# Performance work log

Hardware: AMD Instinct MI355X
Metric: run time of the kernel (lower is better)

The kernel has to match this reference:

```python
import jax, jax.numpy as jnp
import numpy as np

N_NODES = 10000
N_EDGES = 160000
LN_EPS = 1e-5
BN_EPS = 1e-5


def _leaky(x, slope=0.2):
    return jnp.where(x >= 0, x, slope * x)


def _gat_conv(x, edge_index, W, att_src, att_dst, bias, concat):
    # x: [N, Din]; W: [Din, H*C]; att_*: [H, C]
    H, C = att_src.shape
    h = (x @ W).reshape(-1, H, C)                       # [N, H, C]
    a_src = jnp.einsum('nhc,hc->nh', h, att_src)        # [N, H]
    a_dst = jnp.einsum('nhc,hc->nh', h, att_dst)
    src, dst = edge_index[0], edge_index[1]
    logits = _leaky(a_src[src] + a_dst[dst], 0.2)       # [E, H]
    # segment softmax over incoming edges of each dst node
    m = jax.ops.segment_max(logits, dst, num_segments=N_NODES)
    e = jnp.exp(logits - m[dst])
    denom = jax.ops.segment_sum(e, dst, num_segments=N_NODES)
    alpha = e / denom[dst]                              # [E, H]
    msg = h[src] * alpha[:, :, None]                    # [E, H, C]
    out = jax.ops.segment_sum(msg, dst, num_segments=N_NODES)  # [N, H, C]
    if concat:
        out = out.reshape(-1, H * C)
    else:
        out = out.mean(axis=1)
    return out + bias


def setup_inputs() -> dict:
    key = jax.random.key(0)
    ks = jax.random.split(key, 10)
    d_in, H, C = 128, 8, 64
    W = H * C  # 512
    return {
        'x': jax.random.normal(ks[0], (N_NODES, d_in), jnp.float32),
        'edge_index': jax.random.randint(ks[1], (2, N_EDGES), 0, N_NODES, jnp.int64),
        'ft_W': jax.random.normal(ks[2], (d_in, W), jnp.float32) * (1.0 / np.sqrt(d_in)),
        'ft_b': jnp.zeros((W,), jnp.float32),
        'ln_g': jnp.ones((W,), jnp.float32),
        'ln_b': jnp.zeros((W,), jnp.float32),
        'W1': jax.random.normal(ks[3], (W, H * C), jnp.float32) * (1.0 / np.sqrt(W)),
        'att_src1': jax.random.normal(ks[4], (H, C), jnp.float32) * 0.1,
        'att_dst1': jax.random.normal(ks[5], (H, C), jnp.float32) * 0.1,
        'b1': jnp.zeros((W,), jnp.float32),
        'bn_g': jnp.ones((W,), jnp.float32),
        'bn_b': jnp.zeros((W,), jnp.float32),
        'bn_mean': jnp.zeros((W,), jnp.float32),
        'bn_var': jnp.ones((W,), jnp.float32),
        'W2': jax.random.normal(ks[6], (W, H * 2), jnp.float32) * (1.0 / np.sqrt(W)),
        'att_src2': jax.random.normal(ks[7], (H, 2), jnp.float32) * 0.1,
        'att_dst2': jax.random.normal(ks[8], (H, 2), jnp.float32) * 0.1,
        'b2': jnp.zeros((2,), jnp.float32),
    }


def reference(x, edge_index, ft_W, ft_b, ln_g, ln_b, W1, att_src1, att_dst1, b1,
              bn_g, bn_b, bn_mean, bn_var, W2, att_src2, att_dst2, b2):
    # feature transform: Linear -> LayerNorm -> LeakyReLU(0.2)
    h = x @ ft_W + ft_b
    mu = h.mean(axis=-1, keepdims=True)
    var = h.var(axis=-1, keepdims=True)
    h = (h - mu) * jax.lax.rsqrt(var + LN_EPS) * ln_g + ln_b
    h = _leaky(h, 0.2)
    # GAT layer 1 (concat heads) -> BatchNorm (eval) -> ReLU  (dropout = identity in eval)
    h = _gat_conv(h, edge_index, W1, att_src1, att_dst1, b1, concat=True)
    h = (h - bn_mean) * jax.lax.rsqrt(bn_var + BN_EPS) * bn_g + bn_b
    h = jax.nn.relu(h)
    # GAT layer 2 (mean heads) -> logits [N, 2]
    logits = _gat_conv(h, edge_index, W2, att_src2, att_dst2, b2, concat=False)
    return logits
```

## Files before the change

### kernel.cpp

```cpp
#include <hip/hip_runtime.h>
#include <hip/hip_bf16.h>
#include <math.h>

#define N_NODES 10000
#define N_EDGES 160000
#define DIN 128
#define DW 512
#define NHEAD 8
#define NC 64
#define MPAD 10112
#define GEMM_BLKS 316

typedef unsigned short ushort_t;
typedef __attribute__((ext_vector_type(8))) short bf16x8;
typedef __attribute__((ext_vector_type(8))) unsigned short us8;
typedef __attribute__((ext_vector_type(4))) float f32x4;

__device__ inline ushort_t f2bf(float v) {
    unsigned u = __builtin_bit_cast(unsigned, v);
    return (ushort_t)((u + 0x7fff + ((u >> 16) & 1)) >> 16);
}
__device__ inline float bf2f(ushort_t h) {
    return __builtin_bit_cast(float, (unsigned)h << 16);
}

__device__ __forceinline__ size_t swz_idx(int rb, int r, int kp, int nkt) {
    int kt = kp >> 6, kc = kp & 63;
    return ((size_t)(rb * nkt + kt)) * 8192 + r * 64 + (kc ^ ((r & 7) << 3));
}

__device__ __forceinline__ void gld16(const ushort_t* g, ushort_t* l) {
    __builtin_amdgcn_global_load_lds(
        (const __attribute__((address_space(1))) void*)g,
        (__attribute__((address_space(3))) void*)l, 16, 0, 0);
}

__global__ void k_prep(const float* __restrict__ x, const float* __restrict__ ftW,
                       const float* __restrict__ W1f,
                       ushort_t* __restrict__ Ax, ushort_t* __restrict__ Bx,
                       ushort_t* __restrict__ B1,
                       int* __restrict__ cnt, int* __restrict__ cursor) {
    int bid = blockIdx.x, t = threadIdx.x;
    if (bid < 632) {
        int gid = bid * 256 + t;
        int n = gid >> 4, k0 = (gid & 15) * 8;
        float v[8];
        if (n < N_NODES) {
            #pragma unroll
            for (int u = 0; u < 8; u++) v[u] = x[n * DIN + k0 + u];
        } else {
            #pragma unroll
            for (int u = 0; u < 8; u++) v[u] = 0.f;
        }
        us8 hi, lo;
        #pragma unroll
        for (int u = 0; u < 8; u++) {
            ushort_t h = f2bf(v[u]);
            hi[u] = h;
            lo[u] = f2bf(v[u] - bf2f(h));
        }
        int rb = n >> 7, r = n & 127;
        *(us8*)(Ax + swz_idx(rb, r, k0, 4)) = hi;
        *(us8*)(Ax + swz_idx(rb, r, 128 + k0, 4)) = lo;
    } else if (bid < 888) {
        int i = (bid - 632) * 256 + t;
        int n = i >> 7, k = i & 127;
        ushort_t h = f2bf(ftW[k * DW + n]);
        int cb = n >> 7, rc = n & 127;
        Bx[swz_idx(cb, rc, k, 4)] = h;
        Bx[swz_idx(cb, rc, 128 + k, 4)] = h;
    } else if (bid < 1912) {
        int i = (bid - 888) * 256 + t;
        int n = i >> 9, k = i & 511;
        ushort_t h = f2bf(W1f[k * DW + n]);
        int cb = n >> 7, rc = n & 127;
        B1[swz_idx(cb, rc, k, 16)] = h;
        B1[swz_idx(cb, rc, 512 + k, 16)] = h;
    } else {
        int i = (bid - 1912) * 256 + t;
        if (i < N_NODES) { cnt[i] = 0; cursor[i] = 0; }
    }
}

template<int KT, bool ATT, int EXTRA>
__global__ __launch_bounds__(512, 4) void k_tgemm(const ushort_t* __restrict__ A,
                                                  const ushort_t* __restrict__ Bm,
                                                  float* __restrict__ C,
                                                  ushort_t* __restrict__ Cb,
                                                  const float* __restrict__ asrc,
                                                  const float* __restrict__ adst,
                                                  float* __restrict__ aS,
                                                  float* __restrict__ aD,
                                                  const int* __restrict__ ei,
                                                  int* __restrict__ cnt,
                                                  const int* __restrict__ off,
                                                  int* __restrict__ cursor,
                                                  int* __restrict__ csrc) {
    __shared__ __align__(16) ushort_t As[2][8192];
    __shared__ __align__(16) ushort_t Bs[2][8192];
    int bid = blockIdx.x;
    if (bid >= GEMM_BLKS) {
        int e = (bid - GEMM_BLKS) * 512 + threadIdx.x;
        if (e < N_EDGES) {
            if (EXTRA == 1) {
                atomicAdd(&cnt[ei[N_EDGES + e]], 1);
            } else {
                int d = ei[N_EDGES + e];
                int p = off[d] + atomicAdd(&cursor[d], 1);
                csrc[p] = ei[e];
            }
        }
        return;
    }
    int bx = bid >> 2, by = bid & 3;
    int t = threadIdx.x, w = t >> 6, l = t & 63;
    int lm = l & 15, g = l >> 4;
    int wr = w >> 1, wc = w & 1;
    int rowbase = bx * 128;
    int colbase = by * 128;

    const ushort_t* Abase = A + (size_t)bx * KT * 8192 + t * 8;
    const ushort_t* Bbase = Bm + (size_t)by * KT * 8192 + t * 8;

    f32x4 acc[2][4];
    #pragma unroll
    for (int r = 0; r < 2; r++)
        #pragma unroll
        for (int c = 0; c < 4; c++) acc[r][c] = (f32x4){0.f, 0.f, 0.f, 0.f};

    {
        #pragma unroll
        for (int j = 0; j < 2; ++j) {
            gld16(Abase + j * 4096, &As[0][j * 4096 + t * 8]);
            gld16(Bbase + j * 4096, &Bs[0][j * 4096 + t * 8]);
        }
    }

    int p = 0;
    for (int kt = 0; kt < KT; ++kt) {
        __builtin_amdgcn_s_barrier();
        if (kt + 1 < KT) {
            const ushort_t* ga = Abase + (size_t)(kt + 1) * 8192;
            const ushort_t* gb = Bbase + (size_t)(kt + 1) * 8192;
            #pragma unroll
            for (int j = 0; j < 2; ++j) {
                gld16(ga + j * 4096, &As[p ^ 1][j * 4096 + t * 8]);
                gld16(gb + j * 4096, &Bs[p ^ 1][j * 4096 + t * 8]);
            }
            asm volatile("s_waitcnt vmcnt(4)" ::: "memory");
        } else {
            asm volatile("s_waitcnt vmcnt(0)" ::: "memory");
        }
        __builtin_amdgcn_s_barrier();
        const char* Ap = (const char*)As[p];
        const char* Bp = (const char*)Bs[p];
        #pragma unroll
        for (int ks = 0; ks < 2; ++ks) {
            bf16x8 af[2], bfr[4];
            #pragma unroll
            for (int r = 0; r < 2; ++r) {
                int row = wr * 32 + r * 16 + lm;
                af[r] = *(const bf16x8*)(Ap + row * 128 +
                                         ((ks * 64 + g * 16) ^ ((row & 7) << 4)));
            }
            #pragma unroll
            for (int c = 0; c < 4; ++c) {
                int col = wc * 64 + c * 16 + lm;
                bfr[c] = *(const bf16x8*)(Bp + col * 128 +
                                          ((ks * 64 + g * 16) ^ ((col & 7) << 4)));
            }
            #pragma unroll
            for (int r = 0; r < 2; ++r)
                #pragma unroll
                for (int c = 0; c < 4; ++c)
                    acc[r][c] = __builtin_amdgcn_mfma_f32_16x16x32_bf16(af[r], bfr[c], acc[r][c], 0, 0, 0);
        }
        p ^= 1;
    }

    if (!ATT) {
        #pragma unroll
        for (int r = 0; r < 2; ++r) {
            int row0 = rowbase + wr * 32 + r * 16 + g * 4;
            #pragma unroll
            for (int c = 0; c < 4; ++c) {
                int col = colbase + wc * 64 + c * 16 + lm;
                #pragma unroll
                for (int q = 0; q < 4; ++q)
                    if (row0 + q < N_NODES) C[(size_t)(row0 + q) * DW + col] = acc[r][c][q];
            }
        }
    } else {
        int h = 2 * by + wc;
        float asv[4], adv[4];
        #pragma unroll
        for (int c = 0; c < 4; ++c) {
            asv[c] = asrc[h * NC + c * 16 + lm];
            adv[c] = adst[h * NC + c * 16 + lm];
        }
        #pragma unroll
        for (int r = 0; r < 2; ++r) {
            int row0 = rowbase + wr * 32 + r * 16 + g * 4;
            #pragma unroll
            for (int c = 0; c < 4; ++c) {
                int col = colbase + wc * 64 + c * 16 + lm;
                #pragma unroll
                for (int q = 0; q < 4; ++q)
                    if (row0 + q < N_NODES) Cb[(size_t)(row0 + q) * DW + col] = f2bf(acc[r][c][q]);
            }
            #pragma unroll
            for (int q = 0; q < 4; ++q) {
                float ss = acc[r][0][q] * asv[0] + acc[r][1][q] * asv[1] +
                           acc[r][2][q] * asv[2] + acc[r][3][q] * asv[3];
                float dd = acc[r][0][q] * adv[0] + acc[r][1][q] * adv[1] +
                           acc[r][2][q] * adv[2] + acc[r][3][q] * adv[3];
                #pragma unroll
                for (int m = 1; m < 16; m <<= 1) {
                    ss += __shfl_xor(ss, m, 64);
                    dd += __shfl_xor(dd, m, 64);
                }
                int row = row0 + q;
                if (lm == 0 && row < N_NODES) {
                    aS[row * NHEAD + h] = ss;
                    aD[row * NHEAD + h] = dd;
                }
            }
        }
    }
}

__global__ __launch_bounds__(256) void k_ln_scan(const float* __restrict__ hpre,
                                                 const float* __restrict__ fb,
                                                 const float* __restrict__ g,
                                                 const float* __restrict__ beta,
                                                 ushort_t* __restrict__ h0big,
                                                 const int* __restrict__ cnt,
                                                 int* __restrict__ off) {
    __shared__ int ps[256];
    __shared__ float red[8];
    __shared__ __align__(16) ushort_t st[1024];
    int bid = blockIdx.x, t = threadIdx.x;
    if (bid == MPAD) {
        int base = t * 40;
        int loc[40];
        int s = 0;
        #pragma unroll
        for (int i = 0; i < 40; i++) {
            int idx = base + i;
            int v = idx < N_NODES ? cnt[idx] : 0;
            loc[i] = s; s += v;
        }
        ps[t] = s; __syncthreads();
        for (int o = 1; o < 256; o <<= 1) {
            int v = (t >= o) ? ps[t - o] : 0;
            __syncthreads();
            ps[t] += v;
            __syncthreads();
        }
        int pre = (t > 0) ? ps[t - 1] : 0;
        #pragma unroll
        for (int i = 0; i < 40; i++) {
            int idx = base + i;
            if (idx < N_NODES) off[idx] = pre + loc[i];
        }
        if (t == 255) off[N_NODES] = ps[255];
        return;
    }
    int n = bid;
    int rb = n >> 7, r = n & 127;
    if (n >= N_NODES) {
        if (t < 128) {
            int kp0 = t * 8;
            *(us8*)(h0big + ((size_t)(rb * 16 + (kp0 >> 6))) * 8192 + r * 64 +
                    ((kp0 & 63) ^ ((r & 7) << 3))) = (us8){0,0,0,0,0,0,0,0};
        }
        return;
    }
    float a0 = hpre[(size_t)n * DW + t] + fb[t];
    float a1 = hpre[(size_t)n * DW + t + 256] + fb[t + 256];
    float s = a0 + a1, sq = a0 * a0 + a1 * a1;
    for (int o = 32; o > 0; o >>= 1) { s += __shfl_down(s, o, 64); sq += __shfl_down(sq, o, 64); }
    int wid = t >> 6;
    if ((t & 63) == 0) { red[wid] = s; red[4 + wid] = sq; }
    __syncthreads();
    if (t == 0) {
        float ts = red[0] + red[1] + red[2] + red[3];
        float tq = red[4] + red[5] + red[6] + red[7];
        float mu = ts / DW;
        float var = tq / DW - mu * mu;
        red[0] = mu; red[1] = rsqrtf(var + 1e-5f);
    }
    __syncthreads();
    float mu = red[0], rs = red[1];
    float v0 = (a0 - mu) * rs * g[t] + beta[t];
    float v1 = (a1 - mu) * rs * g[t + 256] + beta[t + 256];
    v0 = v0 >= 0.f ? v0 : 0.2f * v0;
    v1 = v1 >= 0.f ? v1 : 0.2f * v1;
    ushort_t h0_ = f2bf(v0), l0_ = f2bf(v0 - bf2f(h0_));
    ushort_t h1_ = f2bf(v1), l1_ = f2bf(v1 - bf2f(h1_));
    st[t] = h0_;        st[256 + t] = h1_;
    st[512 + t] = l0_;  st[768 + t] = l1_;
    __syncthreads();
    if (t < 128) {
        int kp0 = t * 8;
        *(us8*)(h0big + ((size_t)(rb * 16 + (kp0 >> 6))) * 8192 + r * 64 +
                ((kp0 & 63) ^ ((r & 7) << 3))) = *(const us8*)(st + kp0);
    }
}

__global__ __launch_bounds__(256) void k_agg1csr(
    const int* __restrict__ csrc, const int* __restrict__ off,
    const ushort_t* __restrict__ h1b,
    const float* __restrict__ aS, const float* __restrict__ aD,
    const float* __restrict__ b1, const float* __restrict__ bnm,
    const float* __restrict__ bnv, const float* __restrict__ bng,
    const float* __restrict__ bnb, ushort_t* __restrict__ h2b)
{
    int n = blockIdx.x, t = threadIdx.x;
    int beg = off[n], end = off[n + 1];
    __shared__ float wls[64][NHEAD];
    __shared__ int   sls[64];
    __shared__ float aDn[NHEAD];
    __shared__ float dsum[NHEAD];
    if (t < NHEAD) { aDn[t] = aD[n * NHEAD + t]; dsum[t] = 0.f; }
    __syncthreads();
    float acc0 = 0.f, acc1 = 0.f, dpart = 0.f;
    int hA = t >> 5;
    for (int c = beg; c < end; c += 64) {
        int m = min(64, end - c);
        if (t < m) sls[t] = csrc[c + t];
        __syncthreads();
        for (int idx = t; idx < m * NHEAD; idx += 256) {
            int el = idx >> 3, h = idx & 7;
            float l = aS[sls[el] * NHEAD + h] + aDn[h];
            l = l >= 0.f ? l : 0.2f * l;
            float w = __expf(l);
            wls[el][h] = w;
            dpart += w;
        }
        __syncthreads();
        for (int el = 0; el < m; el++) {
            float w = wls[el][hA];
            unsigned v = *(const unsigned*)(h1b + (size_t)sls[el] * DW + 2 * t);
            acc0 += w * __builtin_bit_cast(float, v << 16);
            acc1 += w * __builtin_bit_cast(float, v & 0xffff0000u);
        }
        __syncthreads();
    }
    for (int o = 8; o < 64; o <<= 1) dpart += __shfl_down(dpart, o, 64);
    if ((t & 63) < NHEAD) atomicAdd(&dsum[t & 7], dpart);
    __syncthreads();
    float rd = dsum[hA] > 0.f ? 1.f / dsum[hA] : 0.f;
    int j0 = 2 * t, j1 = 2 * t + 1;
    float v0 = acc0 * rd + b1[j0];
    v0 = (v0 - bnm[j0]) * rsqrtf(bnv[j0] + 1e-5f) * bng[j0] + bnb[j0];
    v0 = v0 > 0.f ? v0 : 0.f;
    float v1 = acc1 * rd + b1[j1];
    v1 = (v1 - bnm[j1]) * rsqrtf(bnv[j1] + 1e-5f) * bng[j1] + bnb[j1];
    v1 = v1 > 0.f ? v1 : 0.f;
    unsigned pk = (unsigned)f2bf(v0) | ((unsigned)f2bf(v1) << 16);
    *(unsigned*)(h2b + (size_t)n * DW + 2 * t) = pk;
}

__global__ __launch_bounds__(256) void k_gemm2att(const ushort_t* __restrict__ h2b,
                                                  const float* __restrict__ W2,
                                                  const float* __restrict__ as2,
                                                  const float* __restrict__ ad2,
                                                  float* __restrict__ gout,
                                                  float* __restrict__ aS,
                                                  float* __restrict__ aD) {
    __shared__ float Ws[DW * 16];
    __shared__ float gl[16][16];
    __shared__ float a2[32];
    int t = threadIdx.x;
    for (int i = t; i < DW * 16; i += 256) Ws[i] = W2[i];
    if (t < 16) a2[t] = as2[t];
    else if (t < 32) a2[t] = ad2[t - 16];
    __syncthreads();
    int nb = blockIdx.x * 16;
    int nl = t >> 4, j = t & 15;
    const bf16x8* hr = (const bf16x8*)(h2b + (size_t)(nb + nl) * DW);
    float acc = 0.f;
    for (int ks = 0; ks < DW / 8; ks++) {
        bf16x8 v = hr[ks];
        #pragma unroll
        for (int u = 0; u < 8; u++)
            acc += bf2f((ushort_t)v[u]) * Ws[(ks * 8 + u) * 16 + j];
    }
    gout[(nb + nl) * 16 + j] = acc;
    gl[nl][j] = acc;
    __syncthreads();
    if (j < 8) {
        aS[(nb + nl) * NHEAD + j] = gl[nl][2 * j] * a2[2 * j] + gl[nl][2 * j + 1] * a2[2 * j + 1];
    } else {
        int h = j - 8;
        aD[(nb + nl) * NHEAD + h] = gl[nl][2 * h] * a2[16 + 2 * h] + gl[nl][2 * h + 1] * a2[16 + 2 * h + 1];
    }
}

__global__ __launch_bounds__(256) void k_agg2csr(
    const int* __restrict__ csrc, const int* __restrict__ off,
    const float* __restrict__ gbuf,
    const float* __restrict__ aS, const float* __restrict__ aD,
    const float* __restrict__ b2, float* __restrict__ outp)
{
    int t = threadIdx.x;
    int n = blockIdx.x * 4 + (t >> 6);
    int lane = t & 63;
    if (n >= N_NODES) return;
    int beg = off[n], end = off[n + 1];
    int j = lane & 15, slot = lane >> 4, h = j >> 1;
    float adn = aD[n * NHEAD + h];
    float acc = 0.f, den = 0.f;
    for (int c = beg + slot; c < end; c += 4) {
        int s = csrc[c];
        float l = aS[s * NHEAD + h] + adn;
        l = l >= 0.f ? l : 0.2f * l;
        float w = __expf(l);
        den += w;
        acc += w * gbuf[s * 16 + j];
    }
    acc += __shfl_down(acc, 16, 64); acc += __shfl_down(acc, 32, 64);
    den += __shfl_down(den, 16, 64); den += __shfl_down(den, 32, 64);
    float v = (lane < 16 && den > 0.f) ? acc / den : 0.f;
    v += __shfl_down(v, 2, 64);
    v += __shfl_down(v, 4, 64);
    v += __shfl_down(v, 8, 64);
    if (lane < 2) outp[n * 2 + lane] = v * 0.125f + b2[lane];
}

extern "C" void kernel_launch(void* const* d_in, const int* in_sizes, int n_in,
                              void* d_out, int out_size, void* d_ws, size_t ws_size,
                              hipStream_t stream) {
    const float* x    = (const float*)d_in[0];
    const int*   ei   = (const int*)d_in[1];
    const float* ftW  = (const float*)d_in[2];
    const float* ftb  = (const float*)d_in[3];
    const float* lng  = (const float*)d_in[4];
    const float* lnb  = (const float*)d_in[5];
    const float* W1   = (const float*)d_in[6];
    const float* as1  = (const float*)d_in[7];
    const float* ad1  = (const float*)d_in[8];
    const float* b1   = (const float*)d_in[9];
    const float* bng  = (const float*)d_in[10];
    const float* bnb  = (const float*)d_in[11];
    const float* bnm  = (const float*)d_in[12];
    const float* bnv  = (const float*)d_in[13];
    const float* W2   = (const float*)d_in[14];
    const float* as2  = (const float*)d_in[15];
    const float* ad2  = (const float*)d_in[16];
    const float* b2   = (const float*)d_in[17];
    float* out = (float*)d_out;

    float* F = (float*)d_ws;
    ushort_t* Ax    = (ushort_t*)(F + 0);
    float*    gbuf  = F + 0;
    ushort_t* Bx    = (ushort_t*)(F + 1294336);
    ushort_t* B1    = (ushort_t*)(F + 1359872);
    float*    hpre  = F + 1622016;
    ushort_t* h2b   = (ushort_t*)(F + 1622016);
    ushort_t* h0big = (ushort_t*)(F + 6799360);
    ushort_t* h1b   = (ushort_t*)(F + 11976704);
    float*    aS1   = F + 14536704;
    float*    aD1   = F + 14616704;
    int* cnt        = (int*)(F + 14696704);
    int* cursor     = (int*)(F + 14706704);
    int* off        = (int*)(F + 14716704);
    int* csrc       = (int*)(F + 14726705);

    k_prep<<<1952, 256, 0, stream>>>(x, ftW, W1, Ax, Bx, B1, cnt, cursor);
    k_tgemm<4, false, 1><<<GEMM_BLKS + 313, 512, 0, stream>>>(
        Ax, Bx, hpre, nullptr, nullptr, nullptr, nullptr, nullptr,
        ei, cnt, nullptr, nullptr, nullptr);
    k_ln_scan<<<MPAD + 1, 256, 0, stream>>>(hpre, ftb, lng, lnb, h0big, cnt, off);
    k_tgemm<16, true, 2><<<GEMM_BLKS + 313, 512, 0, stream>>>(
        h0big, B1, nullptr, h1b, as1, ad1, aS1, aD1,
        ei, nullptr, off, cursor, csrc);
    k_agg1csr<<<N_NODES, 256, 0, stream>>>(csrc, off, h1b, aS1, aD1, b1, bnm, bnv, bng, bnb, h2b);
    k_gemm2att<<<N_NODES / 16, 256, 0, stream>>>(h2b, W2, as2, ad2, gbuf, aS1, aD1);
    k_agg2csr<<<(N_NODES + 3) / 4, 256, 0, stream>>>(csrc, off, gbuf, aS1, aD1, b2, out);
}
```

Baseline: 126.1 us.

## Fuse layer-2 projection and attention scores into layer-1 aggregation kernel

```diff
diff --git a/kernel.cpp b/kernel.cpp
--- a/kernel.cpp
+++ b/kernel.cpp
@@ -271,8 +271,7 @@
     if (n >= N_NODES) {
         if (t < 128) {
             int kp0 = t * 8;
-            *(us8*)(h0big + ((size_t)(rb * 16 + (kp0 >> 6))) * 8192 + r * 64 +
-                    ((kp0 & 63) ^ ((r & 7) << 3))) = (us8){0,0,0,0,0,0,0,0};
+            *(us8*)(h0big + swz_idx(rb, r, kp0, 16)) = (us8){0,0,0,0,0,0,0,0};
         }
         return;
     }
@@ -303,18 +302,20 @@
     __syncthreads();
     if (t < 128) {
         int kp0 = t * 8;
-        *(us8*)(h0big + ((size_t)(rb * 16 + (kp0 >> 6))) * 8192 + r * 64 +
-                ((kp0 & 63) ^ ((r & 7) << 3))) = *(const us8*)(st + kp0);
-    }
-}
-
-__global__ __launch_bounds__(256) void k_agg1csr(
+        *(us8*)(h0big + swz_idx(rb, r, kp0, 16)) = *(const us8*)(st + kp0);
+    }
+}
+
+__global__ __launch_bounds__(256) void k_agg1g2(
     const int* __restrict__ csrc, const int* __restrict__ off,
     const ushort_t* __restrict__ h1b,
     const float* __restrict__ aS, const float* __restrict__ aD,
     const float* __restrict__ b1, const float* __restrict__ bnm,
     const float* __restrict__ bnv, const float* __restrict__ bng,
-    const float* __restrict__ bnb, ushort_t* __restrict__ h2b)
+    const float* __restrict__ bnb,
+    const float* __restrict__ W2, const float* __restrict__ as2,
+    const float* __restrict__ ad2,
+    float* __restrict__ gbuf, float* __restrict__ aS2, float* __restrict__ aD2)
 {
     int n = blockIdx.x, t = threadIdx.x;
     int beg = off[n], end = off[n + 1];
@@ -322,6 +323,9 @@
     __shared__ int   sls[64];
     __shared__ float aDn[NHEAD];
     __shared__ float dsum[NHEAD];
+    __shared__ float h2row[DW];
+    __shared__ float pr[16][17];
+    __shared__ float gl[16];
     if (t < NHEAD) { aDn[t] = aD[n * NHEAD + t]; dsum[t] = 0.f; }
     __syncthreads();
     float acc0 = 0.f, acc1 = 0.f, dpart = 0.f;
@@ -358,43 +362,29 @@
     float v1 = acc1 * rd + b1[j1];
     v1 = (v1 - bnm[j1]) * rsqrtf(bnv[j1] + 1e-5f) * bng[j1] + bnb[j1];
     v1 = v1 > 0.f ? v1 : 0.f;
-    unsigned pk = (unsigned)f2bf(v0) | ((unsigned)f2bf(v1) << 16);
-    *(unsigned*)(h2b + (size_t)n * DW + 2 * t) = pk;
-}
-
-__global__ __launch_bounds__(256) void k_gemm2att(const ushort_t* __restrict__ h2b,
-                                                  const float* __restrict__ W2,
-                                                  const float* __restrict__ as2,
-                                                  const float* __restrict__ ad2,
-                                                  float* __restrict__ gout,
-                                                  float* __restrict__ aS,
-                                                  float* __restrict__ aD) {
-    __shared__ float Ws[DW * 16];
-    __shared__ float gl[16][16];
-    __shared__ float a2[32];
-    int t = threadIdx.x;
-    for (int i = t; i < DW * 16; i += 256) Ws[i] = W2[i];
-    if (t < 16) a2[t] = as2[t];
-    else if (t < 32) a2[t] = ad2[t - 16];
-    __syncthreads();
-    int nb = blockIdx.x * 16;
-    int nl = t >> 4, j = t & 15;
-    const bf16x8* hr = (const bf16x8*)(h2b + (size_t)(nb + nl) * DW);
-    float acc = 0.f;
-    for (int ks = 0; ks < DW / 8; ks++) {
-        bf16x8 v = hr[ks];
-        #pragma unroll
-        for (int u = 0; u < 8; u++)
-            acc += bf2f((ushort_t)v[u]) * Ws[(ks * 8 + u) * 16 + j];
-    }
-    gout[(nb + nl) * 16 + j] = acc;
-    gl[nl][j] = acc;
-    __syncthreads();
-    if (j < 8) {
-        aS[(nb + nl) * NHEAD + j] = gl[nl][2 * j] * a2[2 * j] + gl[nl][2 * j + 1] * a2[2 * j + 1];
-    } else {
-        int h = j - 8;
-        aD[(nb + nl) * NHEAD + h] = gl[nl][2 * h] * a2[16 + 2 * h] + gl[nl][2 * h + 1] * a2[16 + 2 * h + 1];
+    h2row[j0] = v0;
+    h2row[j1] = v1;
+    __syncthreads();
+    int j = t & 15, seg = t >> 4;
+    const float* wp = W2 + (seg * 32) * 16 + j;
+    float part = 0.f;
+    #pragma unroll 8
+    for (int k = 0; k < 32; k++) part += h2row[seg * 32 + k] * wp[k * 16];
+    pr[seg][j] = part;
+    __syncthreads();
+    if (t < 16) {
+        float accg = 0.f;
+        #pragma unroll
+        for (int s2 = 0; s2 < 16; s2++) accg += pr[s2][t];
+        gl[t] = accg;
+        gbuf[n * 16 + t] = accg;
+    }
+    __syncthreads();
+    if (t < 8) {
+        aS2[n * NHEAD + t] = gl[2 * t] * as2[2 * t] + gl[2 * t + 1] * as2[2 * t + 1];
+    } else if (t < 16) {
+        int h = t - 8;
+        aD2[n * NHEAD + h] = gl[2 * h] * ad2[2 * h] + gl[2 * h + 1] * ad2[2 * h + 1];
     }
 }
 
@@ -458,15 +448,16 @@
     ushort_t* Bx    = (ushort_t*)(F + 1294336);
     ushort_t* B1    = (ushort_t*)(F + 1359872);
     float*    hpre  = F + 1622016;
-    ushort_t* h2b   = (ushort_t*)(F + 1622016);
     ushort_t* h0big = (ushort_t*)(F + 6799360);
     ushort_t* h1b   = (ushort_t*)(F + 11976704);
     float*    aS1   = F + 14536704;
     float*    aD1   = F + 14616704;
-    int* cnt        = (int*)(F + 14696704);
-    int* cursor     = (int*)(F + 14706704);
-    int* off        = (int*)(F + 14716704);
-    int* csrc       = (int*)(F + 14726705);
+    float*    aS2   = F + 14696704;
+    float*    aD2   = F + 14776704;
+    int* cnt        = (int*)(F + 14856704);
+    int* cursor     = (int*)(F + 14866704);
+    int* off        = (int*)(F + 14876704);
+    int* csrc       = (int*)(F + 14886705);
 
     k_prep<<<1952, 256, 0, stream>>>(x, ftW, W1, Ax, Bx, B1, cnt, cursor);
     k_tgemm<4, false, 1><<<GEMM_BLKS + 313, 512, 0, stream>>>(
@@ -476,7 +467,8 @@
     k_tgemm<16, true, 2><<<GEMM_BLKS + 313, 512, 0, stream>>>(
         h0big, B1, nullptr, h1b, as1, ad1, aS1, aD1,
         ei, nullptr, off, cursor, csrc);
-    k_agg1csr<<<N_NODES, 256, 0, stream>>>(csrc, off, h1b, aS1, aD1, b1, bnm, bnv, bng, bnb, h2b);
-    k_gemm2att<<<N_NODES / 16, 256, 0, stream>>>(h2b, W2, as2, ad2, gbuf, aS1, aD1);
-    k_agg2csr<<<(N_NODES + 3) / 4, 256, 0, stream>>>(csrc, off, gbuf, aS1, aD1, b2, out);
-}
+    k_agg1g2<<<N_NODES, 256, 0, stream>>>(csrc, off, h1b, aS1, aD1,
+                                          b1, bnm, bnv, bng, bnb,
+                                          W2, as2, ad2, gbuf, aS2, aD2);
+    k_agg2csr<<<(N_NODES + 3) / 4, 256, 0, stream>>>(csrc, off, gbuf, aS2, aD2, b2, out);
+}
```

Measured after the change: 120.5 us. 1.05x faster.

## Split layer-1 aggregation per head with edge-parallel slots per node group

Applied to the files above, without the earlier changes.

```diff
diff --git a/kernel.cpp b/kernel.cpp
--- a/kernel.cpp
+++ b/kernel.cpp
@@ -271,8 +271,7 @@
     if (n >= N_NODES) {
         if (t < 128) {
             int kp0 = t * 8;
-            *(us8*)(h0big + ((size_t)(rb * 16 + (kp0 >> 6))) * 8192 + r * 64 +
-                    ((kp0 & 63) ^ ((r & 7) << 3))) = (us8){0,0,0,0,0,0,0,0};
+            *(us8*)(h0big + swz_idx(rb, r, kp0, 16)) = (us8){0,0,0,0,0,0,0,0};
         }
         return;
     }
@@ -303,12 +302,11 @@
     __syncthreads();
     if (t < 128) {
         int kp0 = t * 8;
-        *(us8*)(h0big + ((size_t)(rb * 16 + (kp0 >> 6))) * 8192 + r * 64 +
-                ((kp0 & 63) ^ ((r & 7) << 3))) = *(const us8*)(st + kp0);
-    }
-}
-
-__global__ __launch_bounds__(256) void k_agg1csr(
+        *(us8*)(h0big + swz_idx(rb, r, kp0, 16)) = *(const us8*)(st + kp0);
+    }
+}
+
+__global__ __launch_bounds__(256) void k_agg1slice(
     const int* __restrict__ csrc, const int* __restrict__ off,
     const ushort_t* __restrict__ h1b,
     const float* __restrict__ aS, const float* __restrict__ aD,
@@ -316,50 +314,50 @@
     const float* __restrict__ bnv, const float* __restrict__ bng,
     const float* __restrict__ bnb, ushort_t* __restrict__ h2b)
 {
-    int n = blockIdx.x, t = threadIdx.x;
-    int beg = off[n], end = off[n + 1];
-    __shared__ float wls[64][NHEAD];
-    __shared__ int   sls[64];
-    __shared__ float aDn[NHEAD];
-    __shared__ float dsum[NHEAD];
-    if (t < NHEAD) { aDn[t] = aD[n * NHEAD + t]; dsum[t] = 0.f; }
-    __syncthreads();
-    float acc0 = 0.f, acc1 = 0.f, dpart = 0.f;
-    int hA = t >> 5;
-    for (int c = beg; c < end; c += 64) {
-        int m = min(64, end - c);
-        if (t < m) sls[t] = csrc[c + t];
-        __syncthreads();
-        for (int idx = t; idx < m * NHEAD; idx += 256) {
-            int el = idx >> 3, h = idx & 7;
-            float l = aS[sls[el] * NHEAD + h] + aDn[h];
+    int bid = blockIdx.x, t = threadIdx.x;
+    int h = bid & 7, ng = bid >> 3;
+    int lane32 = t & 31, slot = t >> 5;
+    int j = h * NC + lane32 * 2;
+    float b10 = b1[j], b11 = b1[j + 1];
+    float sc0 = rsqrtf(bnv[j] + 1e-5f) * bng[j];
+    float sc1 = rsqrtf(bnv[j + 1] + 1e-5f) * bng[j + 1];
+    float mn0 = bnm[j], mn1 = bnm[j + 1];
+    float bb0 = bnb[j], bb1 = bnb[j + 1];
+    __shared__ float red[8][32][2];
+    __shared__ float dred[8];
+    for (int i = 0; i < 8; i++) {
+        int n = ng * 8 + i;
+        int beg = off[n], end = off[n + 1];
+        float adn = aD[n * NHEAD + h];
+        float acc0 = 0.f, acc1 = 0.f, den = 0.f;
+        for (int c = beg + slot; c < end; c += 8) {
+            int src = csrc[c];
+            float l = aS[src * NHEAD + h] + adn;
             l = l >= 0.f ? l : 0.2f * l;
             float w = __expf(l);
-            wls[el][h] = w;
-            dpart += w;
-        }
-        __syncthreads();
-        for (int el = 0; el < m; el++) {
-            float w = wls[el][hA];
-            unsigned v = *(const unsigned*)(h1b + (size_t)sls[el] * DW + 2 * t);
+            den += w;
+            unsigned v = *(const unsigned*)(h1b + (size_t)src * DW + j);
             acc0 += w * __builtin_bit_cast(float, v << 16);
             acc1 += w * __builtin_bit_cast(float, v & 0xffff0000u);
         }
+        if (slot) { red[slot][lane32][0] = acc0; red[slot][lane32][1] = acc1; }
+        if (lane32 == 0) dred[slot] = den;
         __syncthreads();
-    }
-    for (int o = 8; o < 64; o <<= 1) dpart += __shfl_down(dpart, o, 64);
-    if ((t & 63) < NHEAD) atomicAdd(&dsum[t & 7], dpart);
-    __syncthreads();
-    float rd = dsum[hA] > 0.f ? 1.f / dsum[hA] : 0.f;
-    int j0 = 2 * t, j1 = 2 * t + 1;
-    float v0 = acc0 * rd + b1[j0];
-    v0 = (v0 - bnm[j0]) * rsqrtf(bnv[j0] + 1e-5f) * bng[j0] + bnb[j0];
-    v0 = v0 > 0.f ? v0 : 0.f;
-    float v1 = acc1 * rd + b1[j1];
-    v1 = (v1 - bnm[j1]) * rsqrtf(bnv[j1] + 1e-5f) * bng[j1] + bnb[j1];
-    v1 = v1 > 0.f ? v1 : 0.f;
-    unsigned pk = (unsigned)f2bf(v0) | ((unsigned)f2bf(v1) << 16);
-    *(unsigned*)(h2b + (size_t)n * DW + 2 * t) = pk;
+        if (slot == 0) {
+            #pragma unroll
+            for (int s = 1; s < 8; s++) { acc0 += red[s][lane32][0]; acc1 += red[s][lane32][1]; }
+            float dtot = dred[0] + dred[1] + dred[2] + dred[3] +
+                         dred[4] + dred[5] + dred[6] + dred[7];
+            float rd = dtot > 0.f ? 1.f / dtot : 0.f;
+            float v0 = (acc0 * rd + b10 - mn0) * sc0 + bb0;
+            v0 = v0 > 0.f ? v0 : 0.f;
+            float v1 = (acc1 * rd + b11 - mn1) * sc1 + bb1;
+            v1 = v1 > 0.f ? v1 : 0.f;
+            unsigned pk = (unsigned)f2bf(v0) | ((unsigned)f2bf(v1) << 16);
+            *(unsigned*)(h2b + (size_t)n * DW + j) = pk;
+        }
+        __syncthreads();
+    }
 }
 
 __global__ __launch_bounds__(256) void k_gemm2att(const ushort_t* __restrict__ h2b,
@@ -463,10 +461,12 @@
     ushort_t* h1b   = (ushort_t*)(F + 11976704);
     float*    aS1   = F + 14536704;
     float*    aD1   = F + 14616704;
-    int* cnt        = (int*)(F + 14696704);
-    int* cursor     = (int*)(F + 14706704);
-    int* off        = (int*)(F + 14716704);
-    int* csrc       = (int*)(F + 14726705);
+    float*    aS2   = F + 14696704;
+    float*    aD2   = F + 14776704;
+    int* cnt        = (int*)(F + 14856704);
+    int* cursor     = (int*)(F + 14866704);
+    int* off        = (int*)(F + 14876704);
+    int* csrc       = (int*)(F + 14886705);
 
     k_prep<<<1952, 256, 0, stream>>>(x, ftW, W1, Ax, Bx, B1, cnt, cursor);
     k_tgemm<4, false, 1><<<GEMM_BLKS + 313, 512, 0, stream>>>(
@@ -476,7 +476,8 @@
     k_tgemm<16, true, 2><<<GEMM_BLKS + 313, 512, 0, stream>>>(
         h0big, B1, nullptr, h1b, as1, ad1, aS1, aD1,
         ei, nullptr, off, cursor, csrc);
-    k_agg1csr<<<N_NODES, 256, 0, stream>>>(csrc, off, h1b, aS1, aD1, b1, bnm, bnv, bng, bnb, h2b);
-    k_gemm2att<<<N_NODES / 16, 256, 0, stream>>>(h2b, W2, as2, ad2, gbuf, aS1, aD1);
-    k_agg2csr<<<(N_NODES + 3) / 4, 256, 0, stream>>>(csrc, off, gbuf, aS1, aD1, b2, out);
-}
+    k_agg1slice<<<(N_NODES / 8) * 8, 256, 0, stream>>>(
+        csrc, off, h1b, aS1, aD1, b1, bnm, bnv, bng, bnb, h2b);
+    k_gemm2att<<<N_NODES / 16, 256, 0, stream>>>(h2b, W2, as2, ad2, gbuf, aS2, aD2);
+    k_agg2csr<<<(N_NODES + 3) / 4, 256, 0, stream>>>(csrc, off, gbuf, aS2, aD2, b2, out);
+}
```

New measurement: 158.2 us. +25.4%, slower.
